# Performance work log

Hardware: AMD Instinct MI355X
Metric: run time of the kernel (lower is better)

Reference implementation:

```python
import jax, jax.numpy as jnp
import numpy as np
import math

H = 1024          # hidden_size
NUM_LAYERS = 2
V = 32000         # target vocabulary
S = 4096          # source length
W = 64            # window_size
WIN = 2 * W + 1   # max window width (static)
H2 = math.ceil(H / 2)
STD_SQ = (W / 2) ** 2
NEG = -1e30


def setup_inputs() -> dict:
    key = jax.random.key(0)
    ks = jax.random.split(key, 16)
    s = 0.02
    return {
        "source_sentence_length": S,
        "encoder_output": jax.random.normal(ks[0], (S, 1, H), jnp.float32),
        "word": jax.random.randint(ks[1], (1, 1), 0, V),
        "h0": jnp.zeros((NUM_LAYERS, 1, H), jnp.float32),
        "c0": jnp.zeros((NUM_LAYERS, 1, H), jnp.float32),
        "embedding": jax.random.normal(ks[2], (V, H), jnp.float32) * s,
        "lstm_w_ih": jax.random.normal(ks[3], (NUM_LAYERS, 4 * H, H), jnp.float32) * s,
        "lstm_w_hh": jax.random.normal(ks[4], (NUM_LAYERS, 4 * H, H), jnp.float32) * s,
        "lstm_b_ih": jax.random.normal(ks[5], (NUM_LAYERS, 4 * H), jnp.float32) * s,
        "lstm_b_hh": jax.random.normal(ks[6], (NUM_LAYERS, 4 * H), jnp.float32) * s,
        "att_fc1_w": jax.random.normal(ks[7], (H2, H), jnp.float32) * s,
        "att_fc1_b": jax.random.normal(ks[8], (H2,), jnp.float32) * s,
        "att_fc2_w": jax.random.normal(ks[9], (1, H2), jnp.float32) * s,
        "att_fc2_b": jax.random.normal(ks[10], (1,), jnp.float32) * s,
        "fc1_w": jax.random.normal(ks[11], (H, 2 * H), jnp.float32) * s,
        "fc1_b": jax.random.normal(ks[12], (H,), jnp.float32) * s,
        "fc2_w": jax.random.normal(ks[13], (V, H), jnp.float32) * s,
        "fc2_b": jax.random.normal(ks[14], (V,), jnp.float32) * s,
    }


def reference(source_sentence_length, encoder_output, word, h0, c0, embedding,
              lstm_w_ih, lstm_w_hh, lstm_b_ih, lstm_b_hh,
              att_fc1_w, att_fc1_b, att_fc2_w, att_fc2_b,
              fc1_w, fc1_b, fc2_w, fc2_b):
    Sf = jnp.float32(source_sentence_length)
    # embedding lookup (seq=1, batch=1) -> (H,)
    x = embedding[word[0, 0]]
    # stacked LSTM, single time step, torch gate order i,f,g,o
    h_list, c_list = [], []
    for l in range(NUM_LAYERS):
        gates = x @ lstm_w_ih[l].T + lstm_b_ih[l] + h0[l, 0] @ lstm_w_hh[l].T + lstm_b_hh[l]
        i, f, g, o = jnp.split(gates, 4)
        c_new = jax.nn.sigmoid(f) * c0[l, 0] + jax.nn.sigmoid(i) * jnp.tanh(g)
        h_new = jax.nn.sigmoid(o) * jnp.tanh(c_new)
        h_list.append(h_new); c_list.append(c_new)
        x = h_new
    h_n = jnp.stack(h_list)[:, None, :]  # (L,1,H)
    c_n = jnp.stack(c_list)[:, None, :]
    h_t = x  # (H,) decoder output at this step
    # ---- dynamic Gaussian-windowed attention ----
    p = Sf * jax.nn.sigmoid(jnp.tanh(h_t @ att_fc1_w.T + att_fc1_b) @ att_fc2_w.T + att_fc2_b)
    p = p.reshape(())
    ws = jnp.round(jnp.clip(p - W, 0, None)).astype(jnp.int32)                      # clamp(min=0)
    we = jnp.round(jnp.clip(p + W, None, source_sentence_length - 1)).astype(jnp.int32)  # clamp(max=S-1)
    idx = ws + jnp.arange(WIN, dtype=jnp.int32)          # fixed-width window
    valid = idx <= we                                    # replicates [ws:we+1] slice
    h_s = encoder_output[jnp.clip(idx, 0, source_sentence_length - 1), 0, :]
    scores = jnp.where(valid, h_s @ h_t, NEG)
    a = jax.nn.softmax(scores)                           # softmax over window
    gauss = jnp.exp((idx.astype(jnp.float32) - p) / (2.0 * STD_SQ))
    a = jnp.where(valid, a * gauss, 0.0)
    ctx = a @ h_s                                        # (H,)
    # ---- output MLP ----
    out = jnp.tanh(jnp.concatenate([ctx, h_t]) @ fc1_w.T + fc1_b)
    y = jax.nn.log_softmax(out @ fc2_w.T + fc2_b)
    return (y.reshape(1, 1, V), out.reshape(1, 1, H), h_n, c_n, a.reshape(1, 1, WIN))
```

## Files before the change

### kernel.cpp

```cpp
#include <hip/hip_runtime.h>

#define HDIM 1024
#define H4   4096
#define VD   32000
#define WINN 129
#define NEGV (-1e30f)

#define X_    0
#define G_    5120
#define ATT1_ 9216
#define CAT_  9728
#define A_    11776
#define SC_   11908
#define IW_   11912
#define PART_ 12000
#define LOG_  12288

#define O_Y   0
#define O_OUT 32000
#define O_HN  33024
#define O_CN  35072
#define O_A   37120

__device__ __forceinline__ float wred(float v){
  #pragma unroll
  for(int off=32; off; off>>=1) v += __shfl_xor(v, off, 64);
  return v;
}
__device__ __forceinline__ float wmax(float v){
  #pragma unroll
  for(int off=32; off; off>>=1) v = fmaxf(v, __shfl_xor(v, off, 64));
  return v;
}
__device__ __forceinline__ float sigf(float x){ return 1.f/(1.f+expf(-x)); }
__device__ __forceinline__ float dot4(float4 a, float4 b){
  return a.x*b.x + a.y*b.y + a.z*b.z + a.w*b.w;
}


__global__ __launch_bounds__(256) void k_lstm_gemv(
    const float* __restrict__ wih, const float* __restrict__ whh,
    const float* __restrict__ bih, const float* __restrict__ bhh,
    const float* __restrict__ xin, const int* __restrict__ word,
    const float* __restrict__ emb, const float* __restrict__ hin,
    float* __restrict__ gout){
  int gid = blockIdx.x*256 + threadIdx.x;
  int r = gid >> 6, lane = gid & 63;
  const float* xp = word ? (emb + ((size_t)word[0]<<10)) : xin;
  const float* wi = wih + ((size_t)r<<10);
  const float* wh = whh + ((size_t)r<<10);
  float acc = 0.f;
  #pragma unroll
  for (int j=0; j<4; j++){
    int o = lane*4 + 256*j;
    acc += dot4(*(const float4*)(wi+o), *(const float4*)(xp+o));
    acc += dot4(*(const float4*)(wh+o), *(const float4*)(hin+o));
  }
  acc = wred(acc);
  if (lane==0) gout[r] = acc + bih[r] + bhh[r];
}

__global__ __launch_bounds__(256) void k_lstm_act(
    const float* __restrict__ g, const float* __restrict__ c0l,
    float* __restrict__ ws, float* __restrict__ hn, float* __restrict__ cn, int last){
  int j = blockIdx.x*256 + threadIdx.x;
  float gi = g[j], gf = g[1024+j], gg = g[2048+j], go = g[3072+j];
  float c  = sigf(gf)*c0l[j] + sigf(gi)*tanhf(gg);
  float h  = sigf(go)*tanhf(c);
  ws[X_ + j] = h;
  if (last) ws[CAT_ + HDIM + j] = h;
  hn[j] = h;
  cn[j] = c;
}

__global__ __launch_bounds__(256) void k_att1(const float* __restrict__ w,
    const float* __restrict__ b, float* __restrict__ ws){
  int gid = blockIdx.x*256 + threadIdx.x;
  int r = gid >> 6, lane = gid & 63;
  const float* wr = w + ((size_t)r<<10);
  float acc = 0.f;
  #pragma unroll
  for (int j=0; j<4; j++){
    int o = lane*4 + 256*j;
    acc += dot4(*(const float4*)(wr+o), *(const float4*)(ws+X_+o));
  }
  acc = wred(acc);
  if (lane==0) ws[ATT1_ + r] = tanhf(acc + b[r]);
}

__global__ __launch_bounds__(256) void k_scores(const float* __restrict__ enc,
    const int* __restrict__ slen, const float* __restrict__ a2w,
    const float* __restrict__ a2b, float* __restrict__ ws){
  int t = threadIdx.x;
  int lane = t & 63;
  float pacc = 0.f;
  #pragma unroll
  for (int j=0; j<2; j++){
    int o = lane*4 + 256*j;
    pacc += dot4(*(const float4*)(a2w+o), *(const float4*)(ws+ATT1_+o));
  }
  pacc = wred(pacc);
  float Sf = (float)slen[0];
  float p  = Sf * sigf(pacc + a2b[0]);
  int wsi = (int)rintf(fmaxf(p - 64.f, 0.f));
  int wei = (int)rintf(fminf(p + 64.f, Sf - 1.f));
  if (blockIdx.x==0 && t==0){
    ws[SC_] = p;
    ((int*)ws)[IW_]   = wsi;
    ((int*)ws)[IW_+1] = wei;
  }
  int k = blockIdx.x*4 + (t>>6);
  if (k >= WINN) return;
  int idx = wsi + k;
  int smax = slen[0]-1;
  int ci = idx > smax ? smax : (idx < 0 ? 0 : idx);
  const float* er = enc + ((size_t)ci<<10);
  float acc = 0.f;
  #pragma unroll
  for (int j=0; j<4; j++){
    int o = lane*4 + 256*j;
    acc += dot4(*(const float4*)(er+o), *(const float4*)(ws+X_+o));
  }
  acc = wred(acc);
  if (lane==0) ws[A_ + k] = (idx <= wei) ? acc : NEGV;
}

__global__ __launch_bounds__(1024) void k_smctx(const float* __restrict__ enc,
    const int* __restrict__ slen, float* __restrict__ ws, float* __restrict__ aout){
  __shared__ float sarr[WINN];
  __shared__ float av[WINN];
  __shared__ int   ci[WINN];
  __shared__ float red[2];
  int t = threadIdx.x;
  float p = ws[SC_];
  int wsi = ((int*)ws)[IW_], wei = ((int*)ws)[IW_+1];
  int smax = slen[0]-1;
  if (t < WINN){
    sarr[t] = ws[A_ + t];
    int idx = wsi + t;
    ci[t] = idx > smax ? smax : (idx < 0 ? 0 : idx);
  }
  __syncthreads();
  if (t < 64){
    float m = fmaxf(sarr[t], sarr[t+64]);
    if (t==0) m = fmaxf(m, sarr[128]);
    m = wmax(m);
    if (t==0) red[0] = m;
  }
  __syncthreads();
  float M = red[0];
  if (t < 64){
    float e = expf(sarr[t]-M) + expf(sarr[t+64]-M);
    if (t==0) e += expf(sarr[128]-M);
    e = wred(e);
    if (t==0) red[1] = e;
  }
  __syncthreads();
  float sm = red[1];
  if (t < WINN){
    int idx = wsi + t;
    float a = expf(sarr[t]-M) / sm;
    a = (idx <= wei) ? a * expf(((float)idx - p) * (1.f/2048.f)) : 0.f;
    av[t] = a;
    aout[t] = a;
  }
  __syncthreads();
  float acc = 0.f;
  for (int k=0; k<WINN; k++) acc += av[k] * enc[((size_t)ci[k]<<10) + t];
  ws[CAT_ + t] = acc;
}

__global__ __launch_bounds__(256) void k_fc1(const float* __restrict__ w,
    const float* __restrict__ b, float* __restrict__ ws, float* __restrict__ oout){
  int gid = blockIdx.x*256 + threadIdx.x;
  int r = gid >> 6, lane = gid & 63;
  const float* wr = w + ((size_t)r<<11);
  float acc = 0.f;
  #pragma unroll
  for (int j=0; j<8; j++){
    int o = lane*4 + 256*j;
    acc += dot4(*(const float4*)(wr+o), *(const float4*)(ws+CAT_+o));
  }
  acc = wred(acc);
  if (lane==0){
    float o = tanhf(acc + b[r]);
    ws[X_ + r] = o;
    oout[r] = o;
  }
}

__global__ __launch_bounds__(512) void k_fc2(const float* __restrict__ w,
    const float* __restrict__ b, float* __restrict__ ws){
  int gid = blockIdx.x*512 + threadIdx.x;
  int r = gid >> 6, lane = gid & 63;
  const float* wr = w + ((size_t)r<<10);
  float acc = 0.f;
  #pragma unroll
  for (int j=0; j<4; j++){
    int o = lane*4 + 256*j;
    acc += dot4(*(const float4*)(wr+o), *(const float4*)(ws+X_+o));
  }
  acc = wred(acc);
  if (lane==0) ws[LOG_ + r] = acc + b[r];
}

__global__ __launch_bounds__(256) void k_lsepart(float* __restrict__ ws){
  __shared__ float red[4];
  int b = blockIdx.x, t = threadIdx.x;
  int base = b*1024;
  int n = (b==31) ? 256 : 1024;
  bool act = (t*4 < n);
  float4 v = make_float4(0.f,0.f,0.f,0.f);
  if (act) v = *(const float4*)(ws + LOG_ + base + t*4);
  float m = act ? fmaxf(fmaxf(v.x,v.y), fmaxf(v.z,v.w)) : -INFINITY;
  m = wmax(m);
  if ((t&63)==0) red[t>>6] = m;
  __syncthreads();
  float M = fmaxf(fmaxf(red[0],red[1]), fmaxf(red[2],red[3]));
  __syncthreads();
  float s = act ? (expf(v.x-M)+expf(v.y-M)+expf(v.z-M)+expf(v.w-M)) : 0.f;
  s = wred(s);
  if ((t&63)==0) red[t>>6] = s;
  __syncthreads();
  if (t==0){
    ws[PART_ + b]      = M;
    ws[PART_ + 32 + b] = red[0]+red[1]+red[2]+red[3];
  }
}

__global__ __launch_bounds__(256) void k_y(const float* __restrict__ ws, float* __restrict__ y){
  int i = blockIdx.x*256 + threadIdx.x;
  float M = -INFINITY;
  #pragma unroll
  for (int k=0; k<32; k++) M = fmaxf(M, ws[PART_+k]);
  float S = 0.f;
  #pragma unroll
  for (int k=0; k<32; k++) S += ws[PART_+32+k] * expf(ws[PART_+k] - M);
  float off = M + logf(S);
  if (i < 8000){
    float4 v = *(const float4*)(ws + LOG_ + i*4);
    v.x -= off; v.y -= off; v.z -= off; v.w -= off;
    *(float4*)(y + i*4) = v;
  }
}

extern "C" void kernel_launch(void* const* d_in, const int* in_sizes, int n_in,
                              void* d_out, int out_size, void* d_ws, size_t ws_size,
                              hipStream_t stream) {
  const int*   slen = (const int*)d_in[0];
  const float* enc  = (const float*)d_in[1];
  const int*   word = (const int*)d_in[2];
  const float* h0   = (const float*)d_in[3];
  const float* c0   = (const float*)d_in[4];
  const float* emb  = (const float*)d_in[5];
  const float* wih  = (const float*)d_in[6];
  const float* whh  = (const float*)d_in[7];
  const float* bih  = (const float*)d_in[8];
  const float* bhh  = (const float*)d_in[9];
  const float* a1w  = (const float*)d_in[10];
  const float* a1b  = (const float*)d_in[11];
  const float* a2w  = (const float*)d_in[12];
  const float* a2b  = (const float*)d_in[13];
  const float* f1w  = (const float*)d_in[14];
  const float* f1b  = (const float*)d_in[15];
  const float* f2w  = (const float*)d_in[16];
  const float* f2b  = (const float*)d_in[17];
  float* ws  = (float*)d_ws;
  float* out = (float*)d_out;

  k_lstm_gemv<<<1024,256,0,stream>>>(wih, whh, bih, bhh,
                                     nullptr, word, emb, h0, ws + G_);
  k_lstm_act<<<4,256,0,stream>>>(ws + G_, c0, ws, out + O_HN, out + O_CN, 0);
  k_lstm_gemv<<<1024,256,0,stream>>>(wih + (size_t)H4*HDIM, whh + (size_t)H4*HDIM,
                                     bih + H4, bhh + H4,
                                     ws + X_, nullptr, nullptr, h0 + HDIM, ws + G_);
  k_lstm_act<<<4,256,0,stream>>>(ws + G_, c0 + HDIM, ws, out + O_HN + HDIM, out + O_CN + HDIM, 1);

  k_att1<<<128,256,0,stream>>>(a1w, a1b, ws);
  k_scores<<<33,256,0,stream>>>(enc, slen, a2w, a2b, ws);
  k_smctx<<<1,1024,0,stream>>>(enc, slen, ws, out + O_A);
  k_fc1<<<256,256,0,stream>>>(f1w, f1b, ws, out + O_OUT);
  k_fc2<<<4000,512,0,stream>>>(f2w, f2b, ws);
  k_lsepart<<<32,256,0,stream>>>(ws);
  k_y<<<32,256,0,stream>>>(ws, out + O_Y);
}
```

Baseline: 361.9 us.

## Fuse all decoder stages into one cooperative persistent kernel with grid syncs

```diff
diff --git a/kernel.cpp b/kernel.cpp
--- a/kernel.cpp
+++ b/kernel.cpp
@@ -1,4 +1,6 @@
 #include <hip/hip_runtime.h>
+#include <hip/hip_cooperative_groups.h>
+namespace cg = cooperative_groups;
 
 #define HDIM 1024
 #define H4   4096
@@ -7,14 +9,15 @@
 #define NEGV (-1e30f)
 
 #define X_    0
-#define G_    5120
-#define ATT1_ 9216
-#define CAT_  9728
-#define A_    11776
-#define SC_   11908
-#define IW_   11912
-#define PART_ 12000
-#define LOG_  12288
+#define G_    2048
+#define ATT1_ 6144
+#define CAT_  8192
+#define A_    10240
+#define SC_   10376
+#define IW_   10380
+#define PM_   10496
+#define PS_   12544
+#define LOG_  16384
 
 #define O_Y   0
 #define O_OUT 32000
@@ -37,210 +40,255 @@
   return a.x*b.x + a.y*b.y + a.z*b.z + a.w*b.w;
 }
 
-
-__global__ __launch_bounds__(256) void k_lstm_gemv(
+__global__ __launch_bounds__(512) void k_all(
+    const int* __restrict__ slen, const float* __restrict__ enc,
+    const int* __restrict__ word, const float* __restrict__ h0,
+    const float* __restrict__ c0, const float* __restrict__ emb,
     const float* __restrict__ wih, const float* __restrict__ whh,
     const float* __restrict__ bih, const float* __restrict__ bhh,
-    const float* __restrict__ xin, const int* __restrict__ word,
-    const float* __restrict__ emb, const float* __restrict__ hin,
-    float* __restrict__ gout){
-  int gid = blockIdx.x*256 + threadIdx.x;
-  int r = gid >> 6, lane = gid & 63;
-  const float* xp = word ? (emb + ((size_t)word[0]<<10)) : xin;
-  const float* wi = wih + ((size_t)r<<10);
-  const float* wh = whh + ((size_t)r<<10);
-  float acc = 0.f;
-  #pragma unroll
-  for (int j=0; j<4; j++){
-    int o = lane*4 + 256*j;
-    acc += dot4(*(const float4*)(wi+o), *(const float4*)(xp+o));
-    acc += dot4(*(const float4*)(wh+o), *(const float4*)(hin+o));
-  }
-  acc = wred(acc);
-  if (lane==0) gout[r] = acc + bih[r] + bhh[r];
-}
-
-__global__ __launch_bounds__(256) void k_lstm_act(
-    const float* __restrict__ g, const float* __restrict__ c0l,
-    float* __restrict__ ws, float* __restrict__ hn, float* __restrict__ cn, int last){
-  int j = blockIdx.x*256 + threadIdx.x;
-  float gi = g[j], gf = g[1024+j], gg = g[2048+j], go = g[3072+j];
-  float c  = sigf(gf)*c0l[j] + sigf(gi)*tanhf(gg);
-  float h  = sigf(go)*tanhf(c);
-  ws[X_ + j] = h;
-  if (last) ws[CAT_ + HDIM + j] = h;
-  hn[j] = h;
-  cn[j] = c;
-}
-
-__global__ __launch_bounds__(256) void k_att1(const float* __restrict__ w,
-    const float* __restrict__ b, float* __restrict__ ws){
-  int gid = blockIdx.x*256 + threadIdx.x;
-  int r = gid >> 6, lane = gid & 63;
-  const float* wr = w + ((size_t)r<<10);
-  float acc = 0.f;
-  #pragma unroll
-  for (int j=0; j<4; j++){
-    int o = lane*4 + 256*j;
-    acc += dot4(*(const float4*)(wr+o), *(const float4*)(ws+X_+o));
-  }
-  acc = wred(acc);
-  if (lane==0) ws[ATT1_ + r] = tanhf(acc + b[r]);
-}
-
-__global__ __launch_bounds__(256) void k_scores(const float* __restrict__ enc,
-    const int* __restrict__ slen, const float* __restrict__ a2w,
-    const float* __restrict__ a2b, float* __restrict__ ws){
-  int t = threadIdx.x;
-  int lane = t & 63;
-  float pacc = 0.f;
-  #pragma unroll
-  for (int j=0; j<2; j++){
-    int o = lane*4 + 256*j;
-    pacc += dot4(*(const float4*)(a2w+o), *(const float4*)(ws+ATT1_+o));
-  }
-  pacc = wred(pacc);
-  float Sf = (float)slen[0];
-  float p  = Sf * sigf(pacc + a2b[0]);
-  int wsi = (int)rintf(fmaxf(p - 64.f, 0.f));
-  int wei = (int)rintf(fminf(p + 64.f, Sf - 1.f));
-  if (blockIdx.x==0 && t==0){
-    ws[SC_] = p;
-    ((int*)ws)[IW_]   = wsi;
-    ((int*)ws)[IW_+1] = wei;
-  }
-  int k = blockIdx.x*4 + (t>>6);
-  if (k >= WINN) return;
-  int idx = wsi + k;
-  int smax = slen[0]-1;
-  int ci = idx > smax ? smax : (idx < 0 ? 0 : idx);
-  const float* er = enc + ((size_t)ci<<10);
-  float acc = 0.f;
-  #pragma unroll
-  for (int j=0; j<4; j++){
-    int o = lane*4 + 256*j;
-    acc += dot4(*(const float4*)(er+o), *(const float4*)(ws+X_+o));
-  }
-  acc = wred(acc);
-  if (lane==0) ws[A_ + k] = (idx <= wei) ? acc : NEGV;
-}
-
-__global__ __launch_bounds__(1024) void k_smctx(const float* __restrict__ enc,
-    const int* __restrict__ slen, float* __restrict__ ws, float* __restrict__ aout){
-  __shared__ float sarr[WINN];
-  __shared__ float av[WINN];
-  __shared__ int   ci[WINN];
-  __shared__ float red[2];
-  int t = threadIdx.x;
-  float p = ws[SC_];
-  int wsi = ((int*)ws)[IW_], wei = ((int*)ws)[IW_+1];
-  int smax = slen[0]-1;
-  if (t < WINN){
-    sarr[t] = ws[A_ + t];
-    int idx = wsi + t;
-    ci[t] = idx > smax ? smax : (idx < 0 ? 0 : idx);
-  }
-  __syncthreads();
-  if (t < 64){
-    float m = fmaxf(sarr[t], sarr[t+64]);
-    if (t==0) m = fmaxf(m, sarr[128]);
-    m = wmax(m);
-    if (t==0) red[0] = m;
-  }
-  __syncthreads();
-  float M = red[0];
-  if (t < 64){
-    float e = expf(sarr[t]-M) + expf(sarr[t+64]-M);
-    if (t==0) e += expf(sarr[128]-M);
-    e = wred(e);
-    if (t==0) red[1] = e;
-  }
-  __syncthreads();
-  float sm = red[1];
-  if (t < WINN){
-    int idx = wsi + t;
-    float a = expf(sarr[t]-M) / sm;
-    a = (idx <= wei) ? a * expf(((float)idx - p) * (1.f/2048.f)) : 0.f;
-    av[t] = a;
-    aout[t] = a;
-  }
-  __syncthreads();
-  float acc = 0.f;
-  for (int k=0; k<WINN; k++) acc += av[k] * enc[((size_t)ci[k]<<10) + t];
-  ws[CAT_ + t] = acc;
-}
-
-__global__ __launch_bounds__(256) void k_fc1(const float* __restrict__ w,
-    const float* __restrict__ b, float* __restrict__ ws, float* __restrict__ oout){
-  int gid = blockIdx.x*256 + threadIdx.x;
-  int r = gid >> 6, lane = gid & 63;
-  const float* wr = w + ((size_t)r<<11);
-  float acc = 0.f;
-  #pragma unroll
-  for (int j=0; j<8; j++){
-    int o = lane*4 + 256*j;
-    acc += dot4(*(const float4*)(wr+o), *(const float4*)(ws+CAT_+o));
-  }
-  acc = wred(acc);
-  if (lane==0){
-    float o = tanhf(acc + b[r]);
-    ws[X_ + r] = o;
-    oout[r] = o;
-  }
-}
-
-__global__ __launch_bounds__(512) void k_fc2(const float* __restrict__ w,
-    const float* __restrict__ b, float* __restrict__ ws){
-  int gid = blockIdx.x*512 + threadIdx.x;
-  int r = gid >> 6, lane = gid & 63;
-  const float* wr = w + ((size_t)r<<10);
-  float acc = 0.f;
-  #pragma unroll
-  for (int j=0; j<4; j++){
-    int o = lane*4 + 256*j;
-    acc += dot4(*(const float4*)(wr+o), *(const float4*)(ws+X_+o));
-  }
-  acc = wred(acc);
-  if (lane==0) ws[LOG_ + r] = acc + b[r];
-}
-
-__global__ __launch_bounds__(256) void k_lsepart(float* __restrict__ ws){
-  __shared__ float red[4];
-  int b = blockIdx.x, t = threadIdx.x;
-  int base = b*1024;
-  int n = (b==31) ? 256 : 1024;
-  bool act = (t*4 < n);
-  float4 v = make_float4(0.f,0.f,0.f,0.f);
-  if (act) v = *(const float4*)(ws + LOG_ + base + t*4);
-  float m = act ? fmaxf(fmaxf(v.x,v.y), fmaxf(v.z,v.w)) : -INFINITY;
-  m = wmax(m);
-  if ((t&63)==0) red[t>>6] = m;
-  __syncthreads();
-  float M = fmaxf(fmaxf(red[0],red[1]), fmaxf(red[2],red[3]));
-  __syncthreads();
-  float s = act ? (expf(v.x-M)+expf(v.y-M)+expf(v.z-M)+expf(v.w-M)) : 0.f;
-  s = wred(s);
-  if ((t&63)==0) red[t>>6] = s;
-  __syncthreads();
-  if (t==0){
-    ws[PART_ + b]      = M;
-    ws[PART_ + 32 + b] = red[0]+red[1]+red[2]+red[3];
-  }
-}
-
-__global__ __launch_bounds__(256) void k_y(const float* __restrict__ ws, float* __restrict__ y){
-  int i = blockIdx.x*256 + threadIdx.x;
-  float M = -INFINITY;
-  #pragma unroll
-  for (int k=0; k<32; k++) M = fmaxf(M, ws[PART_+k]);
-  float S = 0.f;
-  #pragma unroll
-  for (int k=0; k<32; k++) S += ws[PART_+32+k] * expf(ws[PART_+k] - M);
-  float off = M + logf(S);
-  if (i < 8000){
-    float4 v = *(const float4*)(ws + LOG_ + i*4);
-    v.x -= off; v.y -= off; v.z -= off; v.w -= off;
-    *(float4*)(y + i*4) = v;
+    const float* __restrict__ a1w, const float* __restrict__ a1b,
+    const float* __restrict__ a2w, const float* __restrict__ a2b,
+    const float* __restrict__ f1w, const float* __restrict__ f1b,
+    const float* __restrict__ f2w, const float* __restrict__ f2b,
+    float* __restrict__ ws, float* __restrict__ out)
+{
+  cg::grid_group grid = cg::this_grid();
+  const int t    = threadIdx.x;
+  const int gt   = blockIdx.x*512 + t;
+  const int w    = gt >> 6;
+  const int lane = t & 63;
+
+  {
+    const float* xp = emb + ((size_t)word[0]<<10);
+    float4 xv[4], hv[4];
+    #pragma unroll
+    for (int j=0;j<4;j++){ int o = lane*4+256*j; xv[j] = *(const float4*)(xp+o); hv[j] = *(const float4*)(h0+o); }
+    #pragma unroll
+    for (int rr=0; rr<2; rr++){
+      int r = w + rr*2048;
+      const float* wi = wih + ((size_t)r<<10);
+      const float* wh = whh + ((size_t)r<<10);
+      float acc = 0.f;
+      #pragma unroll
+      for (int j=0;j<4;j++){
+        int o = lane*4+256*j;
+        acc += dot4(*(const float4*)(wi+o), xv[j]);
+        acc += dot4(*(const float4*)(wh+o), hv[j]);
+      }
+      acc = wred(acc);
+      if (lane==0) ws[G_+r] = acc + bih[r] + bhh[r];
+    }
+  }
+  grid.sync();
+  if (gt < 1024){
+    float gi = ws[G_+gt], gf = ws[G_+1024+gt], gg = ws[G_+2048+gt], go = ws[G_+3072+gt];
+    float c = sigf(gf)*c0[gt] + sigf(gi)*tanhf(gg);
+    float h = sigf(go)*tanhf(c);
+    ws[X_+gt] = h;
+    out[O_HN+gt] = h; out[O_CN+gt] = c;
+  }
+  grid.sync();
+  {
+    const float* hin = h0 + HDIM;
+    float4 xv[4], hv[4];
+    #pragma unroll
+    for (int j=0;j<4;j++){ int o = lane*4+256*j; xv[j] = *(const float4*)(ws+X_+o); hv[j] = *(const float4*)(hin+o); }
+    #pragma unroll
+    for (int rr=0; rr<2; rr++){
+      int r = w + rr*2048;
+      const float* wi = wih + (size_t)H4*HDIM + ((size_t)r<<10);
+      const float* wh = whh + (size_t)H4*HDIM + ((size_t)r<<10);
+      float acc = 0.f;
+      #pragma unroll
+      for (int j=0;j<4;j++){
+        int o = lane*4+256*j;
+        acc += dot4(*(const float4*)(wi+o), xv[j]);
+        acc += dot4(*(const float4*)(wh+o), hv[j]);
+      }
+      acc = wred(acc);
+      if (lane==0) ws[G_+r] = acc + bih[H4+r] + bhh[H4+r];
+    }
+  }
+  grid.sync();
+  if (gt < 1024){
+    float gi = ws[G_+gt], gf = ws[G_+1024+gt], gg = ws[G_+2048+gt], go = ws[G_+3072+gt];
+    float c = sigf(gf)*c0[HDIM+gt] + sigf(gi)*tanhf(gg);
+    float h = sigf(go)*tanhf(c);
+    ws[X_+gt] = h;
+    ws[CAT_+HDIM+gt] = h;
+    out[O_HN+HDIM+gt] = h; out[O_CN+HDIM+gt] = c;
+  }
+  grid.sync();
+  if (w < 512){
+    const float* wr = a1w + ((size_t)w<<10);
+    float acc = 0.f;
+    #pragma unroll
+    for (int j=0;j<4;j++){
+      int o = lane*4+256*j;
+      acc += dot4(*(const float4*)(wr+o), *(const float4*)(ws+X_+o));
+    }
+    acc = wred(acc);
+    if (lane==0) ws[ATT1_+w] = tanhf(acc + a1b[w]);
+  }
+  grid.sync();
+  if (w < WINN){
+    float pacc = 0.f;
+    #pragma unroll
+    for (int j=0;j<2;j++){
+      int o = lane*4+256*j;
+      pacc += dot4(*(const float4*)(a2w+o), *(const float4*)(ws+ATT1_+o));
+    }
+    pacc = wred(pacc);
+    float Sf = (float)slen[0];
+    float p  = Sf * sigf(pacc + a2b[0]);
+    int wsi = (int)rintf(fmaxf(p - 64.f, 0.f));
+    int wei = (int)rintf(fminf(p + 64.f, Sf - 1.f));
+    if (w==0 && lane==0){
+      ws[SC_] = p;
+      ((int*)ws)[IW_] = wsi; ((int*)ws)[IW_+1] = wei;
+    }
+    int idx = wsi + w;
+    int smax = slen[0]-1;
+    int ci = idx > smax ? smax : (idx < 0 ? 0 : idx);
+    const float* er = enc + ((size_t)ci<<10);
+    float acc = 0.f;
+    #pragma unroll
+    for (int j=0;j<4;j++){
+      int o = lane*4+256*j;
+      acc += dot4(*(const float4*)(er+o), *(const float4*)(ws+X_+o));
+    }
+    acc = wred(acc);
+    if (lane==0) ws[A_+w] = (idx <= wei) ? acc : NEGV;
+  }
+  grid.sync();
+  {
+    __shared__ float sarr[WINN];
+    __shared__ float av[WINN];
+    __shared__ int   cis[WINN];
+    __shared__ float red2[2];
+    float p = ws[SC_];
+    int wsi = ((int*)ws)[IW_], wei = ((int*)ws)[IW_+1];
+    int smax = slen[0]-1;
+    if (t < WINN){
+      sarr[t] = ws[A_+t];
+      int idx = wsi + t;
+      cis[t] = idx > smax ? smax : (idx < 0 ? 0 : idx);
+    }
+    __syncthreads();
+    if (t < 64){
+      float m = fmaxf(sarr[t], sarr[t+64]);
+      if (t==0) m = fmaxf(m, sarr[128]);
+      m = wmax(m);
+      if (t==0) red2[0] = m;
+    }
+    __syncthreads();
+    float M = red2[0];
+    if (t < 64){
+      float e = expf(sarr[t]-M) + expf(sarr[t+64]-M);
+      if (t==0) e += expf(sarr[128]-M);
+      e = wred(e);
+      if (t==0) red2[1] = e;
+    }
+    __syncthreads();
+    float sm = red2[1];
+    if (t < WINN){
+      int idx = wsi + t;
+      float a = expf(sarr[t]-M) / sm;
+      a = (idx <= wei) ? a * expf(((float)idx - p) * (1.f/2048.f)) : 0.f;
+      av[t] = a;
+      if (blockIdx.x==0) out[O_A+t] = a;
+    }
+    __syncthreads();
+    int v = t >> 6;
+    if (v < 4){
+      int i = blockIdx.x*4 + v;
+      float acc = av[lane]      * enc[((size_t)cis[lane]<<10) + i]
+                + av[lane+64]   * enc[((size_t)cis[lane+64]<<10) + i];
+      if (lane==0) acc += av[128] * enc[((size_t)cis[128]<<10) + i];
+      acc = wred(acc);
+      if (lane==0) ws[CAT_+i] = acc;
+    }
+  }
+  grid.sync();
+  if (w < 1024){
+    const float* wr = f1w + ((size_t)w<<11);
+    float acc = 0.f;
+    #pragma unroll
+    for (int j=0;j<8;j++){
+      int o = lane*4+256*j;
+      acc += dot4(*(const float4*)(wr+o), *(const float4*)(ws+CAT_+o));
+    }
+    acc = wred(acc);
+    if (lane==0){
+      float o = tanhf(acc + f1b[w]);
+      ws[X_+w] = o;
+      out[O_OUT+w] = o;
+    }
+  }
+  grid.sync();
+  {
+    float4 xv[4];
+    #pragma unroll
+    for (int j=0;j<4;j++){ int o = lane*4+256*j; xv[j] = *(const float4*)(ws+X_+o); }
+    float mw = -INFINITY, sw = 0.f;
+    #pragma unroll 4
+    for (int j=0;j<16;j++){
+      int r = w + 2048*j;
+      if (r < VD){
+        const float* wr = f2w + ((size_t)r<<10);
+        float acc = 0.f;
+        #pragma unroll
+        for (int jj=0;jj<4;jj++){
+          int o = lane*4+256*jj;
+          acc += dot4(*(const float4*)(wr+o), xv[jj]);
+        }
+        acc = wred(acc);
+        float v = acc + f2b[r];
+        if (lane==0) ws[LOG_+r] = v;
+        float mn = fmaxf(mw, v);
+        sw = sw*expf(mw-mn) + expf(v-mn);
+        mw = mn;
+      }
+    }
+    if (lane==0){ ws[PM_+w] = mw; ws[PS_+w] = sw; }
+  }
+  grid.sync();
+  if (blockIdx.x==0){
+    __shared__ float pm[8], ps[8];
+    float m = -INFINITY, s = 0.f;
+    for (int k=t; k<2048; k+=512){
+      float mk = ws[PM_+k], sk = ws[PS_+k];
+      float mn = fmaxf(m, mk);
+      s = s*expf(m-mn) + sk*expf(mk-mn);
+      m = mn;
+    }
+    #pragma unroll
+    for (int off=32; off; off>>=1){
+      float mo = __shfl_xor(m, off, 64), so = __shfl_xor(s, off, 64);
+      float mn = fmaxf(m, mo);
+      s = s*expf(m-mn) + so*expf(mo-mn);
+      m = mn;
+    }
+    if (lane==0){ pm[t>>6] = m; ps[t>>6] = s; }
+    __syncthreads();
+    if (t==0){
+      float M = pm[0], S = ps[0];
+      for (int k=1;k<8;k++){
+        float mn = fmaxf(M, pm[k]);
+        S = S*expf(M-mn) + ps[k]*expf(pm[k]-mn);
+        M = mn;
+      }
+      ws[SC_+1] = M + logf(S);
+    }
+  }
+  grid.sync();
+  {
+    float off = ws[SC_+1];
+    if (gt < 8000){
+      float4 v = *(const float4*)(ws + LOG_ + gt*4);
+      v.x -= off; v.y -= off; v.z -= off; v.w -= off;
+      *(float4*)(out + O_Y + gt*4) = v;
+    }
   }
 }
 
@@ -268,19 +316,10 @@
   float* ws  = (float*)d_ws;
   float* out = (float*)d_out;
 
-  k_lstm_gemv<<<1024,256,0,stream>>>(wih, whh, bih, bhh,
-                                     nullptr, word, emb, h0, ws + G_);
-  k_lstm_act<<<4,256,0,stream>>>(ws + G_, c0, ws, out + O_HN, out + O_CN, 0);
-  k_lstm_gemv<<<1024,256,0,stream>>>(wih + (size_t)H4*HDIM, whh + (size_t)H4*HDIM,
-                                     bih + H4, bhh + H4,
-                                     ws + X_, nullptr, nullptr, h0 + HDIM, ws + G_);
-  k_lstm_act<<<4,256,0,stream>>>(ws + G_, c0 + HDIM, ws, out + O_HN + HDIM, out + O_CN + HDIM, 1);
-
-  k_att1<<<128,256,0,stream>>>(a1w, a1b, ws);
-  k_scores<<<33,256,0,stream>>>(enc, slen, a2w, a2b, ws);
-  k_smctx<<<1,1024,0,stream>>>(enc, slen, ws, out + O_A);
-  k_fc1<<<256,256,0,stream>>>(f1w, f1b, ws, out + O_OUT);
-  k_fc2<<<4000,512,0,stream>>>(f2w, f2b, ws);
-  k_lsepart<<<32,256,0,stream>>>(ws);
-  k_y<<<32,256,0,stream>>>(ws, out + O_Y);
-}
+  void* args[] = { (void*)&slen, (void*)&enc, (void*)&word, (void*)&h0, (void*)&c0,
+                   (void*)&emb, (void*)&wih, (void*)&whh, (void*)&bih, (void*)&bhh,
+                   (void*)&a1w, (void*)&a1b, (void*)&a2w, (void*)&a2b,
+                   (void*)&f1w, (void*)&f1b, (void*)&f2w, (void*)&f2b,
+                   (void*)&ws, (void*)&out };
+  hipLaunchCooperativeKernel((void*)k_all, dim3(256), dim3(512), args, 0, stream);
+}
```

New measurement: 633.9 us. 1.75x slower.
